# Performance work log

Measured on AMD Instinct MI355X. Metric: run time of the kernel, lower is better.

The kernel has to match this reference:

```python
import jax, jax.numpy as jnp
import numpy as np

R = 64
NF = 128
NUM_RNA = 4000
NUM_DIS = 2000
N_GLOBAL = 16
N_NODE = NUM_RNA + NUM_DIS + N_GLOBAL
E = 300000
P = 500000
MLP_DIMS = [(2 * R, R), (R, R // 2), (R // 2, 32), (32, 16), (16, 8), (8, 1)]


def _xavier(k, shape):
    fan_in = shape[0]
    fan_out = shape[-1]
    lim = float(np.sqrt(6.0 / (fan_in + fan_out)))
    return jax.random.uniform(k, shape, jnp.float32, -lim, lim)


def setup_inputs() -> dict:
    key = jax.random.key(0)
    ks = jax.random.split(key, 32)
    inp = {}
    inp["x"] = jax.random.normal(ks[0], (N_NODE, NF), jnp.float32)
    inp["adj"] = jax.random.randint(ks[1], (2, E), 0, N_NODE)
    inp["coo"] = jax.random.randint(ks[2], (P, 2), 0, NUM_DIS)
    dims = [NF, R]
    for i in range(2):
        inp[f"gw{i}"] = _xavier(ks[3 + 4 * i], (dims[i], R))
        inp[f"gas{i}"] = _xavier(ks[4 + 4 * i], (R,))
        inp[f"gad{i}"] = _xavier(ks[5 + 4 * i], (R,))
        inp[f"gb{i}"] = jnp.zeros((R,), jnp.float32)
    for j, (di, do) in enumerate(MLP_DIMS, start=1):
        inp[f"w{j}"] = _xavier(ks[12 + 2 * j], (di, do))
        inp[f"b{j}"] = jnp.zeros((do,), jnp.float32)
    return inp


def _gat_layer(x, src, dst, W, a_src, a_dst, b):
    # PyG GATConv, heads=1, add_self_loops handled by caller, negative_slope=0.2
    n = x.shape[0]
    h = x @ W                                    # [n, R]
    e = jax.nn.leaky_relu((h * a_src).sum(-1)[src] + (h * a_dst).sum(-1)[dst], 0.2)
    m = jax.ops.segment_max(e, dst, num_segments=n)
    ex = jnp.exp(e - m[dst])
    denom = jax.ops.segment_sum(ex, dst, num_segments=n)
    alpha = ex / denom[dst]                      # softmax over incoming edges
    return jax.ops.segment_sum(alpha[:, None] * h[src], dst, num_segments=n) + b


def reference(x, adj, coo, gw0, gas0, gad0, gb0, gw1, gas1, gad1, gb1,
              w1, b1, w2, b2, w3, b3, w4, b4, w5, b5, w6, b6):
    n = x.shape[0]
    loop = jnp.arange(n)
    src = jnp.concatenate([adj[0], loop])        # add self loops (GATConv default)
    dst = jnp.concatenate([adj[1], loop])
    h = _gat_layer(x, src, dst, gw0, gas0, gad0, gb0)
    h = _gat_layer(h, src, dst, gw1, gas1, gad1, gb1)
    x1 = h[:NUM_RNA]
    x2 = h[NUM_RNA:NUM_RNA + NUM_DIS]
    # vectorized per-pair gather + concat (original loops in python)
    z = jnp.concatenate([x1[coo[:, 0]], x2[coo[:, 1]]], axis=1)  # [P, 2R]
    for w, b in ((w1, b1), (w2, b2), (w3, b3), (w4, b4), (w5, b5)):
        z = jax.nn.relu(z @ w + b)
    return jax.nn.sigmoid(z @ w6 + b6)           # [P, 1]
```

## Files before the change

kernel.cpp:

```cpp
#include <hip/hip_runtime.h>
#include <cstdint>

#define N_RNA 4000
#define N_DIS 2000
#define NNODE 6016
#define NFDIM 128
#define RDIM 64
#define NE 300000
#define NET (NE + NNODE)
#define NPAIR 500000
#define NTILE (NPAIR / 16)
#define MAXD 128
#define FILLB 1196
#define PROJB (NNODE / 16)

typedef float vf4 __attribute__((ext_vector_type(4)));
typedef _Float16 f16x8 __attribute__((ext_vector_type(8)));
typedef _Float16 f16x2 __attribute__((ext_vector_type(2)));

union FragU {
    f16x8 f;
    f16x2 h[4];
    int   u[4];
    uint4 q;
};

__device__ __forceinline__ f16x2 pkrtz(float lo, float hi) {
    auto r = __builtin_amdgcn_cvt_pkrtz(lo, hi);
    return __builtin_bit_cast(f16x2, r);
}
__device__ __forceinline__ vf4 mfma16(const FragU& a, const FragU& b, vf4 c) {
    return __builtin_amdgcn_mfma_f32_16x16x32_f16(a.f, b.f, c, 0, 0, 0);
}
__device__ __forceinline__ unsigned addrelu2(unsigned a, unsigned b) {
    f16x2 x = __builtin_bit_cast(f16x2, a) + __builtin_bit_cast(f16x2, b);
    f16x2 zz = {(_Float16)0.f, (_Float16)0.f};
    x = __builtin_elementwise_max(x, zz);
    return __builtin_bit_cast(unsigned, x);
}

__device__ __forceinline__ FragU trans16(vf4 a, int col, int g) {
    int w0, w1;
    {
        f16x2 p0 = pkrtz(a[0], a[1]);
        f16x2 p1 = pkrtz(a[2], a[3]);
        FragU tmp; tmp.h[0] = p0; tmp.h[1] = p1;
        w0 = tmp.u[0]; w1 = tmp.u[1];
    }
    int addrA = (col + 16 * ((2 * g) & 3)) * 4;
    int addrB = (col + 16 * ((2 * g + 1) & 3)) * 4;
    int j0 = __builtin_amdgcn_ds_bpermute(addrA, w0);
    int j1 = __builtin_amdgcn_ds_bpermute(addrA, w1);
    int j2 = __builtin_amdgcn_ds_bpermute(addrB, w0);
    int j3 = __builtin_amdgcn_ds_bpermute(addrB, w1);
    bool lo2 = g < 2;
    FragU B;
    B.u[0] = lo2 ? j0 : 0;
    B.u[1] = lo2 ? j1 : 0;
    B.u[2] = lo2 ? j2 : 0;
    B.u[3] = lo2 ? j3 : 0;
    return B;
}

__global__ void setup_kernel(int* __restrict__ cur,
                             const float* __restrict__ w2, const float* __restrict__ w3,
                             const float* __restrict__ w4, const float* __restrict__ w5,
                             uint4* __restrict__ gfrag) {
    int i = blockIdx.x * blockDim.x + threadIdx.x;
    if (i < NNODE) cur[i] = 0;
    if (blockIdx.x == 0 && threadIdx.x < 64) {
        int l = threadIdx.x;
        int rho = l & 15, g = l >> 4;
        int fbase = 8 * (rho >> 2) + (rho & 3);
        FragU F;
#pragma unroll
        for (int t = 0; t < 2; t++)
#pragma unroll
            for (int kt = 0; kt < 2; kt++) {
#pragma unroll
                for (int j = 0; j < 4; j++) {
                    int k = kt * 32 + g * 8 + 2 * j;
                    F.h[j] = pkrtz(w2[k * 32 + fbase + 4 * t],
                                   w2[(k + 1) * 32 + fbase + 4 * t]);
                }
                gfrag[(t * 2 + kt) * 64 + l] = F.q;
            }
#pragma unroll
        for (int t = 0; t < 2; t++) {
#pragma unroll
            for (int j = 0; j < 4; j++) {
                int k = g * 8 + 2 * j;
                F.h[j] = pkrtz(w3[k * 32 + fbase + 4 * t],
                               w3[(k + 1) * 32 + fbase + 4 * t]);
            }
            gfrag[(4 + t) * 64 + l] = F.q;
        }
#pragma unroll
        for (int j = 0; j < 4; j++) {
            int k = g * 8 + 2 * j;
            F.h[j] = pkrtz(w4[k * 16 + rho], w4[(k + 1) * 16 + rho]);
        }
        gfrag[6 * 64 + l] = F.q;
#pragma unroll
        for (int j = 0; j < 4; j++) {
            int k = g * 8 + 2 * j;
            if (g < 2 && rho < 8)
                F.h[j] = pkrtz(w5[k * 8 + rho], w5[(k + 1) * 8 + rho]);
            else
                F.u[j] = 0;
        }
        gfrag[7 * 64 + l] = F.q;
    }
}

__global__ __launch_bounds__(256) void fill_proj_kernel(
    const int* __restrict__ adj, int* __restrict__ cur, int* __restrict__ slots,
    const float* __restrict__ x, const float* __restrict__ W,
    const float* __restrict__ a_s, const float* __restrict__ a_d,
    float* __restrict__ h, float* __restrict__ ssrc, float* __restrict__ sdst) {
    int b = blockIdx.x;
    if (b < FILLB) {
        int k = b * 256 + threadIdx.x;
        if (k >= NET) return;
        int src, dst;
        if (k < NE) { src = adj[k]; dst = adj[NE + k]; }
        else        { src = k - NE; dst = k - NE; }
        int pos = atomicAdd(&cur[dst], 1);
        if (pos < MAXD) slots[dst * MAXD + pos] = src;
        return;
    }
    __shared__ float xr[16][NFDIM];
    int pb = b - FILLB;
    int wv = threadIdx.x >> 6, t = threadIdx.x & 63;
    int nb = pb * 16 + wv * 4;
    for (int idx = t; idx < 4 * NFDIM; idx += 64)
        xr[wv * 4 + idx / NFDIM][idx % NFDIM] = x[(size_t)nb * NFDIM + idx];
    __syncthreads();
    float a0 = 0.f, a1 = 0.f, a2 = 0.f, a3 = 0.f;
#pragma unroll 8
    for (int k = 0; k < NFDIM; k++) {
        float wvv = W[k * RDIM + t];
        a0 = fmaf(xr[wv * 4 + 0][k], wvv, a0);
        a1 = fmaf(xr[wv * 4 + 1][k], wvv, a1);
        a2 = fmaf(xr[wv * 4 + 2][k], wvv, a2);
        a3 = fmaf(xr[wv * 4 + 3][k], wvv, a3);
    }
    h[(size_t)(nb + 0) * RDIM + t] = a0;
    h[(size_t)(nb + 1) * RDIM + t] = a1;
    h[(size_t)(nb + 2) * RDIM + t] = a2;
    h[(size_t)(nb + 3) * RDIM + t] = a3;
    float asv = a_s[t], adv = a_d[t];
    float acc[4] = {a0, a1, a2, a3};
#pragma unroll
    for (int i = 0; i < 4; i++) {
        float vs = acc[i] * asv;
        float vd = acc[i] * adv;
#pragma unroll
        for (int off = 32; off; off >>= 1) {
            vs += __shfl_down(vs, off);
            vd += __shfl_down(vd, off);
        }
        if (t == 0) { ssrc[nb + i] = vs; sdst[nb + i] = vd; }
    }
}

#define AGG_BODY_128(H, SS, SD, BIAS)                                       \
    int deg = cur[node]; if (deg > MAXD) deg = MAXD;                        \
    int beg = node * MAXD, end = beg + deg;                                 \
    float sd = (SD)[node];                                                  \
    int gg = tid >> 3, q8 = tid & 7;                                        \
    float4 A0 = {0.f, 0.f, 0.f, 0.f}, A1 = {0.f, 0.f, 0.f, 0.f};            \
    float den = 0.f;                                                        \
    for (int i = beg + gg; i < end; i += 16) {                              \
        int s = slots[i];                                                   \
        float v = (SS)[s] + sd;                                             \
        v = v > 0.f ? v : 0.2f * v;                                         \
        float ex = __expf(v);                                               \
        den += ex;                                                          \
        const float4* hp = (const float4*)((H) + (size_t)s * 64 + q8 * 8);  \
        float4 h0 = hp[0], h1 = hp[1];                                      \
        A0.x = fmaf(ex, h0.x, A0.x); A0.y = fmaf(ex, h0.y, A0.y);           \
        A0.z = fmaf(ex, h0.z, A0.z); A0.w = fmaf(ex, h0.w, A0.w);           \
        A1.x = fmaf(ex, h1.x, A1.x); A1.y = fmaf(ex, h1.y, A1.y);           \
        A1.z = fmaf(ex, h1.z, A1.z); A1.w = fmaf(ex, h1.w, A1.w);           \
    }                                                                       \
    _Pragma("unroll")                                                       \
    for (int off = 8; off <= 32; off <<= 1) {                               \
        A0.x += __shfl_xor(A0.x, off); A0.y += __shfl_xor(A0.y, off);       \
        A0.z += __shfl_xor(A0.z, off); A0.w += __shfl_xor(A0.w, off);       \
        A1.x += __shfl_xor(A1.x, off); A1.y += __shfl_xor(A1.y, off);       \
        A1.z += __shfl_xor(A1.z, off); A1.w += __shfl_xor(A1.w, off);       \
        den += __shfl_xor(den, off);                                        \
    }                                                                       \
    if (t < 8) {                                                            \
        smA[wv][8 * t + 0] = A0.x; smA[wv][8 * t + 1] = A0.y;               \
        smA[wv][8 * t + 2] = A0.z; smA[wv][8 * t + 3] = A0.w;               \
        smA[wv][8 * t + 4] = A1.x; smA[wv][8 * t + 5] = A1.y;               \
        smA[wv][8 * t + 6] = A1.z; smA[wv][8 * t + 7] = A1.w;               \
        if (t == 0) smD[wv] = den;                                          \
    }                                                                       \
    __syncthreads();                                                        \
    if (wv == 0) {                                                          \
        float inv = 1.f / (smD[0] + smD[1]);                                \
        smf[t] = (smA[0][t] + smA[1][t]) * inv + (BIAS)[t];                 \
    }

__global__ __launch_bounds__(128) void agg_proj_kernel(
    const float* __restrict__ h, const float* __restrict__ ssrc, const float* __restrict__ sdst,
    const int* __restrict__ cur, const int* __restrict__ slots,
    const float* __restrict__ bias,
    const float* __restrict__ W,
    const float* __restrict__ a_s, const float* __restrict__ a_d,
    float* __restrict__ h2, float* __restrict__ ssrc2, float* __restrict__ sdst2) {
    __shared__ float smA[2][64];
    __shared__ float smD[2];
    __shared__ float smf[64];
    int node = blockIdx.x;
    int tid = threadIdx.x;
    int wv = tid >> 6, t = tid & 63;
    AGG_BODY_128(h, ssrc, sdst, bias)
    if (wv == 0) {
        float hv = 0.f;
#pragma unroll 8
        for (int k = 0; k < 64; k++) hv = fmaf(smf[k], W[k * 64 + t], hv);
        h2[(size_t)node * 64 + t] = hv;
        float vs = hv * a_s[t];
        float vd = hv * a_d[t];
#pragma unroll
        for (int off = 32; off; off >>= 1) {
            vs += __shfl_down(vs, off);
            vd += __shfl_down(vd, off);
        }
        if (t == 0) { ssrc2[node] = vs; sdst2[node] = vd; }
    }
}

__global__ __launch_bounds__(128) void agg_pre_kernel(
    const float* __restrict__ h, const float* __restrict__ ssrc, const float* __restrict__ sdst,
    const int* __restrict__ cur, const int* __restrict__ slots,
    const float* __restrict__ bias,
    const float* __restrict__ w1, const float* __restrict__ b1,
    _Float16* __restrict__ u1h, _Float16* __restrict__ u2h) {
    __shared__ float smA[2][64];
    __shared__ float smD[2];
    __shared__ float smf[64];
    int node = blockIdx.x;
    int tid = threadIdx.x;
    int wv = tid >> 6, t = tid & 63;
    AGG_BODY_128(h, ssrc, sdst, bias)
    if (wv == 0) {
        bool rna = node < N_RNA;
        const float* w = rna ? w1 : (w1 + 64 * 64);
        float uk = rna ? b1[t] : 0.f;
#pragma unroll 8
        for (int k = 0; k < 64; k++) uk = fmaf(smf[k], w[k * 64 + t], uk);
        _Float16* dst = rna ? (u1h + (size_t)node * 64) : (u2h + (size_t)(node - N_RNA) * 64);
        dst[t] = (_Float16)uk;
    }
}

__global__ __launch_bounds__(256) void mlp_mfma_kernel(
    const _Float16* __restrict__ u1h, const _Float16* __restrict__ u2h,
    const int* __restrict__ coo, const uint4* __restrict__ gfrag,
    const float* __restrict__ b2, const float* __restrict__ b3,
    const float* __restrict__ b4, const float* __restrict__ b5,
    const float* __restrict__ w6, const float* __restrict__ b6,
    float* __restrict__ out) {
    int tid = threadIdx.x;
    const int lane = tid & 63;
    const int col  = lane & 15;
    const int g    = lane >> 4;
    const int wid  = blockIdx.x * 4 + (tid >> 6);
    const int nwaves = gridDim.x * 4;

    FragU A200, A201, A210, A211, A30, A31, A4f, A5f;
    A200.q = gfrag[0 * 64 + lane];
    A201.q = gfrag[1 * 64 + lane];
    A210.q = gfrag[2 * 64 + lane];
    A211.q = gfrag[3 * 64 + lane];
    A30.q  = gfrag[4 * 64 + lane];
    A31.q  = gfrag[5 * 64 + lane];
    A4f.q  = gfrag[6 * 64 + lane];
    A5f.q  = gfrag[7 * 64 + lane];

    float bias2[8], bias3[8], bias4[4], bias5[4], w6r[4];
#pragma unroll
    for (int i = 0; i < 8; i++) {
        bias2[i] = b2[8 * g + i];
        bias3[i] = b3[8 * g + i];
    }
#pragma unroll
    for (int r = 0; r < 4; r++) {
        bias4[r] = b4[g * 4 + r];
        bias5[r] = (g < 2) ? b5[g * 4 + r] : 0.f;
        w6r[r]   = (g < 2) ? w6[g * 4 + r] : 0.f;
    }
    float b6v = b6[0];
    const vf4 z = {0.f, 0.f, 0.f, 0.f};

    auto chain = [&](uint4 r0, uint4 r1, uint4 d0, uint4 d1) -> float {
        FragU B0, B1;
        B0.u[0] = addrelu2(r0.x, d0.x);
        B0.u[1] = addrelu2(r0.y, d0.y);
        B0.u[2] = addrelu2(r0.z, d0.z);
        B0.u[3] = addrelu2(r0.w, d0.w);
        B1.u[0] = addrelu2(r1.x, d1.x);
        B1.u[1] = addrelu2(r1.y, d1.y);
        B1.u[2] = addrelu2(r1.z, d1.z);
        B1.u[3] = addrelu2(r1.w, d1.w);
        vf4 acc0 = mfma16(A200, B0, z);
        acc0 = mfma16(A201, B1, acc0);
        vf4 acc1 = mfma16(A210, B0, z);
        acc1 = mfma16(A211, B1, acc1);
#pragma unroll
        for (int r = 0; r < 4; r++) {
            acc0[r] = fmaxf(acc0[r] + bias2[r], 0.f);
            acc1[r] = fmaxf(acc1[r] + bias2[4 + r], 0.f);
        }
        FragU Bx;
        Bx.h[0] = pkrtz(acc0[0], acc0[1]);
        Bx.h[1] = pkrtz(acc0[2], acc0[3]);
        Bx.h[2] = pkrtz(acc1[0], acc1[1]);
        Bx.h[3] = pkrtz(acc1[2], acc1[3]);
        acc0 = mfma16(A30, Bx, z);
        acc1 = mfma16(A31, Bx, z);
#pragma unroll
        for (int r = 0; r < 4; r++) {
            acc0[r] = fmaxf(acc0[r] + bias3[r], 0.f);
            acc1[r] = fmaxf(acc1[r] + bias3[4 + r], 0.f);
        }
        Bx.h[0] = pkrtz(acc0[0], acc0[1]);
        Bx.h[1] = pkrtz(acc0[2], acc0[3]);
        Bx.h[2] = pkrtz(acc1[0], acc1[1]);
        Bx.h[3] = pkrtz(acc1[2], acc1[3]);
        vf4 a4 = mfma16(A4f, Bx, z);
#pragma unroll
        for (int r = 0; r < 4; r++) a4[r] = fmaxf(a4[r] + bias4[r], 0.f);
        Bx = trans16(a4, col, g);
        vf4 a5 = mfma16(A5f, Bx, z);
        float part = 0.f;
#pragma unroll
        for (int r = 0; r < 4; r++)
            part = fmaf(fmaxf(a5[r] + bias5[r], 0.f), w6r[r], part);
        part += __shfl_xor(part, 16);
        return 1.f / (1.f + __expf(-(part + b6v)));
    };

    int tile = wid;
    uint4 r0, r1, d0, d1;
    if (tile < NTILE) {
        int p = tile * 16 + col;
        int2 rd = ((const int2*)coo)[p];
        const uint4* pr = (const uint4*)(u1h + (size_t)rd.x * 64);
        const uint4* pd = (const uint4*)(u2h + (size_t)rd.y * 64);
        r0 = pr[g]; r1 = pr[4 + g]; d0 = pd[g]; d1 = pd[4 + g];
    }
    while (tile < NTILE) {
        int next = tile + nwaves;
        uint4 nr0, nr1, nd0, nd1;
        if (next < NTILE) {
            int p = next * 16 + col;
            int2 rd = ((const int2*)coo)[p];
            const uint4* pr = (const uint4*)(u1h + (size_t)rd.x * 64);
            const uint4* pd = (const uint4*)(u2h + (size_t)rd.y * 64);
            nr0 = pr[g]; nr1 = pr[4 + g]; nd0 = pd[g]; nd1 = pd[4 + g];
        }
        float sig = chain(r0, r1, d0, d1);
        if (g == 0) out[tile * 16 + col] = sig;
        tile = next;
        r0 = nr0; r1 = nr1; d0 = nd0; d1 = nd1;
    }
}

extern "C" void kernel_launch(void* const* d_in, const int* in_sizes, int n_in,
                              void* d_out, int out_size, void* d_ws, size_t ws_size,
                              hipStream_t stream) {
    const float* x    = (const float*)d_in[0];
    const int*   adj  = (const int*)d_in[1];
    const int*   coo  = (const int*)d_in[2];
    const float* gw0  = (const float*)d_in[3];
    const float* gas0 = (const float*)d_in[4];
    const float* gad0 = (const float*)d_in[5];
    const float* gb0  = (const float*)d_in[6];
    const float* gw1  = (const float*)d_in[7];
    const float* gas1 = (const float*)d_in[8];
    const float* gad1 = (const float*)d_in[9];
    const float* gb1  = (const float*)d_in[10];

    char* ws = (char*)d_ws;
    size_t o = 0;
    auto take = [&](size_t bytes) -> void* {
        void* p = ws + o;
        o = (o + bytes + 255) & ~(size_t)255;
        return p;
    };
    float*     hP    = (float*)take((size_t)NNODE * RDIM * 4);
    float*     hP2   = (float*)take((size_t)NNODE * RDIM * 4);
    _Float16*  u1h   = (_Float16*)take((size_t)N_RNA * 64 * 2);
    _Float16*  u2h   = (_Float16*)take((size_t)N_DIS * 64 * 2);
    uint4*     gfrag = (uint4*)take((size_t)8 * 64 * 16);
    float*     ssrc  = (float*)take((size_t)NNODE * 4);
    float*     sdst  = (float*)take((size_t)NNODE * 4);
    float*     ssrc2 = (float*)take((size_t)NNODE * 4);
    float*     sdst2 = (float*)take((size_t)NNODE * 4);
    int*       cur   = (int*)take((size_t)NNODE * 4);
    int*       slots = (int*)take((size_t)NNODE * MAXD * 4);

    setup_kernel<<<(NNODE + 255) / 256, 256, 0, stream>>>(
        cur,
        (const float*)d_in[13], (const float*)d_in[15],
        (const float*)d_in[17], (const float*)d_in[19], gfrag);
    fill_proj_kernel<<<FILLB + PROJB, 256, 0, stream>>>(
        adj, cur, slots, x, gw0, gas0, gad0, hP, ssrc, sdst);
    agg_proj_kernel<<<NNODE, 128, 0, stream>>>(hP, ssrc, sdst, cur, slots, gb0,
                                               gw1, gas1, gad1, hP2, ssrc2, sdst2);
    agg_pre_kernel<<<N_RNA + N_DIS, 128, 0, stream>>>(
        hP2, ssrc2, sdst2, cur, slots, gb1,
        (const float*)d_in[11], (const float*)d_in[12], u1h, u2h);
    mlp_mfma_kernel<<<2048, 256, 0, stream>>>(
        u1h, u2h, coo, gfrag,
        (const float*)d_in[14], (const float*)d_in[16],
        (const float*)d_in[18], (const float*)d_in[20],
        (const float*)d_in[21], (const float*)d_in[22],
        (float*)d_out);
}
```

Baseline: 82.39 us.

## Precompute edge weights in shared memory and split projection across both waves

The aggregation now has one thread per incoming edge compute the attention exponent once. It stores the exponent and the source index in shared memory and reduces the denominator up front, so the gather loop only loads features. The following 64x64 projection is split by k-halves across both waves of the block and combined through shared memory, where before only wave 0 did it. This adds extra block barriers per node in exchange for removing redundant exp/index work and idle-wave time.

```diff
diff --git a/kernel.cpp b/kernel.cpp
--- a/kernel.cpp
+++ b/kernel.cpp
@@ -164,19 +164,30 @@
     }
 }
 
-#define AGG_BODY_128(H, SS, SD, BIAS)                                       \
+#define AGG_BODY_V2(H, SS, SD, BIAS)                                        \
     int deg = cur[node]; if (deg > MAXD) deg = MAXD;                        \
-    int beg = node * MAXD, end = beg + deg;                                 \
     float sd = (SD)[node];                                                  \
+    float myex = 0.f;                                                       \
+    if (tid < deg) {                                                        \
+        int s = slots[node * MAXD + tid];                                   \
+        smI[tid] = s;                                                       \
+        float v = (SS)[s] + sd;                                             \
+        v = v > 0.f ? v : 0.2f * v;                                         \
+        myex = __expf(v);                                                   \
+        smS[tid] = myex;                                                    \
+    }                                                                       \
+    float den = myex;                                                       \
+    _Pragma("unroll")                                                       \
+    for (int off = 1; off < 64; off <<= 1) den += __shfl_xor(den, off);     \
+    if (t == 0) smD[wv] = den;                                              \
+    __syncthreads();                                                        \
+    float fullden = smD[0] + smD[1];                                        \
     int gg = tid >> 3, q8 = tid & 7;                                        \
     float4 A0 = {0.f, 0.f, 0.f, 0.f}, A1 = {0.f, 0.f, 0.f, 0.f};            \
-    float den = 0.f;                                                        \
-    for (int i = beg + gg; i < end; i += 16) {                              \
-        int s = slots[i];                                                   \
-        float v = (SS)[s] + sd;                                             \
-        v = v > 0.f ? v : 0.2f * v;                                         \
-        float ex = __expf(v);                                               \
-        den += ex;                                                          \
+    _Pragma("unroll 2")                                                     \
+    for (int i = gg; i < deg; i += 16) {                                    \
+        float ex = smS[i];                                                  \
+        int s = smI[i];                                                     \
         const float4* hp = (const float4*)((H) + (size_t)s * 64 + q8 * 8);  \
         float4 h0 = hp[0], h1 = hp[1];                                      \
         A0.x = fmaf(ex, h0.x, A0.x); A0.y = fmaf(ex, h0.y, A0.y);           \
@@ -190,20 +201,19 @@
         A0.z += __shfl_xor(A0.z, off); A0.w += __shfl_xor(A0.w, off);       \
         A1.x += __shfl_xor(A1.x, off); A1.y += __shfl_xor(A1.y, off);       \
         A1.z += __shfl_xor(A1.z, off); A1.w += __shfl_xor(A1.w, off);       \
-        den += __shfl_xor(den, off);                                        \
     }                                                                       \
     if (t < 8) {                                                            \
         smA[wv][8 * t + 0] = A0.x; smA[wv][8 * t + 1] = A0.y;               \
         smA[wv][8 * t + 2] = A0.z; smA[wv][8 * t + 3] = A0.w;               \
         smA[wv][8 * t + 4] = A1.x; smA[wv][8 * t + 5] = A1.y;               \
         smA[wv][8 * t + 6] = A1.z; smA[wv][8 * t + 7] = A1.w;               \
-        if (t == 0) smD[wv] = den;                                          \
     }                                                                       \
     __syncthreads();                                                        \
     if (wv == 0) {                                                          \
-        float inv = 1.f / (smD[0] + smD[1]);                                \
+        float inv = 1.f / fullden;                                          \
         smf[t] = (smA[0][t] + smA[1][t]) * inv + (BIAS)[t];                 \
-    }
+    }                                                                       \
+    __syncthreads();
 
 __global__ __launch_bounds__(128) void agg_proj_kernel(
     const float* __restrict__ h, const float* __restrict__ ssrc, const float* __restrict__ sdst,
@@ -212,17 +222,24 @@
     const float* __restrict__ W,
     const float* __restrict__ a_s, const float* __restrict__ a_d,
     float* __restrict__ h2, float* __restrict__ ssrc2, float* __restrict__ sdst2) {
+    __shared__ float smS[MAXD];
+    __shared__ int   smI[MAXD];
     __shared__ float smA[2][64];
     __shared__ float smD[2];
     __shared__ float smf[64];
+    __shared__ float smP[64];
     int node = blockIdx.x;
     int tid = threadIdx.x;
     int wv = tid >> 6, t = tid & 63;
-    AGG_BODY_128(h, ssrc, sdst, bias)
+    AGG_BODY_V2(h, ssrc, sdst, bias)
+    float part = 0.f;
+    int k0 = wv * 32;
+#pragma unroll 8
+    for (int k = 0; k < 32; k++) part = fmaf(smf[k0 + k], W[(k0 + k) * 64 + t], part);
+    if (wv == 1) smP[t] = part;
+    __syncthreads();
     if (wv == 0) {
-        float hv = 0.f;
-#pragma unroll 8
-        for (int k = 0; k < 64; k++) hv = fmaf(smf[k], W[k * 64 + t], hv);
+        float hv = part + smP[t];
         h2[(size_t)node * 64 + t] = hv;
         float vs = hv * a_s[t];
         float vd = hv * a_d[t];
@@ -241,19 +258,26 @@
     const float* __restrict__ bias,
     const float* __restrict__ w1, const float* __restrict__ b1,
     _Float16* __restrict__ u1h, _Float16* __restrict__ u2h) {
+    __shared__ float smS[MAXD];
+    __shared__ int   smI[MAXD];
     __shared__ float smA[2][64];
     __shared__ float smD[2];
     __shared__ float smf[64];
+    __shared__ float smP[64];
     int node = blockIdx.x;
     int tid = threadIdx.x;
     int wv = tid >> 6, t = tid & 63;
-    AGG_BODY_128(h, ssrc, sdst, bias)
+    AGG_BODY_V2(h, ssrc, sdst, bias)
+    bool rna = node < N_RNA;
+    const float* w = rna ? w1 : (w1 + 64 * 64);
+    float part = (wv == 0 && rna) ? b1[t] : 0.f;
+    int k0 = wv * 32;
+#pragma unroll 8
+    for (int k = 0; k < 32; k++) part = fmaf(smf[k0 + k], w[(k0 + k) * 64 + t], part);
+    if (wv == 1) smP[t] = part;
+    __syncthreads();
     if (wv == 0) {
-        bool rna = node < N_RNA;
-        const float* w = rna ? w1 : (w1 + 64 * 64);
-        float uk = rna ? b1[t] : 0.f;
-#pragma unroll 8
-        for (int k = 0; k < 64; k++) uk = fmaf(smf[k], w[k * 64 + t], uk);
+        float uk = part + smP[t];
         _Float16* dst = rna ? (u1h + (size_t)node * 64) : (u2h + (size_t)(node - N_RNA) * 64);
         dst[t] = (_Float16)uk;
     }
```

Measured after the change: 79.08 us. -4.0%, faster.
